# Optimization experiments

Measured on AMD Instinct MI355X. Metric: run time of the kernel, lower is better.

Reference implementation:

```python
import jax, jax.numpy as jnp
import numpy as np

NUM_GRAPHS = 256


def _gcn_norm(edge_index, num_nodes):
    # Add self-loops and compute symmetric normalization coeffs (PyG gcn_norm).
    loops = jnp.arange(num_nodes, dtype=edge_index.dtype)
    row = jnp.concatenate([edge_index[0], loops])  # source nodes
    col = jnp.concatenate([edge_index[1], loops])  # target nodes
    deg = jax.ops.segment_sum(jnp.ones_like(col, dtype=jnp.float32), col,
                              num_segments=num_nodes)
    dis = jnp.where(deg > 0, jax.lax.rsqrt(jnp.maximum(deg, 1.0)), 0.0)
    norm = dis[row] * dis[col]  # [E + N]
    return row, col, norm


def _gcn_conv(x, row, col, norm, W, b, num_nodes):
    h = x @ W                                        # [N, out] dense transform first
    msg = norm[:, None] * h[row]                     # gather + scale  [E+N, out]
    out = jax.ops.segment_sum(msg, col, num_segments=num_nodes)  # scatter-add
    return out + b


def setup_inputs() -> dict:
    key = jax.random.key(0)
    k = jax.random.split(key, 12)
    N, E, F_IN, H = 100000, 1600000, 64, 64
    x = jax.random.normal(k[0], (N, F_IN), dtype=jnp.float32)
    edge_index = jax.random.randint(k[1], (2, E), 0, N, dtype=jnp.int64)
    batch_index = jnp.sort(jax.random.randint(k[2], (N,), 0, NUM_GRAPHS, dtype=jnp.int64))
    s = 1.0 / np.sqrt(F_IN)
    W1 = jax.random.uniform(k[3], (F_IN, H), minval=-s, maxval=s, dtype=jnp.float32)
    b1 = jnp.zeros((H,), dtype=jnp.float32)
    W2 = jax.random.uniform(k[4], (H, H), minval=-s, maxval=s, dtype=jnp.float32)
    b2 = jnp.zeros((H,), dtype=jnp.float32)
    Wl1 = jax.random.uniform(k[5], (H, H // 2), minval=-s, maxval=s, dtype=jnp.float32)
    bl1 = jax.random.uniform(k[6], (H // 2,), minval=-s, maxval=s, dtype=jnp.float32)
    Wl2 = jax.random.uniform(k[7], (H // 2, 2), minval=-s, maxval=s, dtype=jnp.float32)
    bl2 = jax.random.uniform(k[8], (2,), minval=-s, maxval=s, dtype=jnp.float32)
    return {"x": x, "edge_index": edge_index, "batch_index": batch_index,
            "W1": W1, "b1": b1, "W2": W2, "b2": b2,
            "Wl1": Wl1, "bl1": bl1, "Wl2": Wl2, "bl2": bl2}


def reference(x, edge_index, batch_index, W1, b1, W2, b2, Wl1, bl1, Wl2, bl2):
    N = x.shape[0]
    row, col, norm = _gcn_norm(edge_index, N)
    h = jax.nn.relu(_gcn_conv(x, row, col, norm, W1, b1, N))
    h = jax.nn.relu(_gcn_conv(h, row, col, norm, W2, b2, N))
    # global mean pool over batch_index
    sums = jax.ops.segment_sum(h, batch_index, num_segments=NUM_GRAPHS)
    cnts = jax.ops.segment_sum(jnp.ones((N,), dtype=h.dtype), batch_index,
                               num_segments=NUM_GRAPHS)
    g = sums / jnp.maximum(cnts, 1.0)[:, None]       # [G, H]
    g = jax.nn.relu(g @ Wl1 + bl1)                    # dropout is identity in eval
    logits = g @ Wl2 + bl2
    return jax.nn.log_softmax(logits, axis=1)
```

## Files before the change

kernel.cpp:

```cpp
#include <hip/hip_runtime.h>
#include <hip/hip_fp8.h>
#include <cstdint>
#include <cstddef>


#define HF 64
#define BSH 8
#define BSZ 256
#define PCHUNK 4096
#define PADB 6144
#define CNTCLAMP (PADB - 4 * BSZ)
#define POISON 0xAAAAAAAAu

typedef unsigned u32;

__device__ __forceinline__ unsigned short f2bf(float x) {
    unsigned u = __float_as_uint(x);
    unsigned r = (u + 0x7fffu + ((u >> 16) & 1u)) >> 16;
    return (unsigned short)r;
}
__device__ __forceinline__ float bfl(u32 w) { return __uint_as_float(w << 16); }
__device__ __forceinline__ float bfh(u32 w) { return __uint_as_float(w & 0xffff0000u); }
__device__ __forceinline__ float bf2f(unsigned short s) { return __uint_as_float(((u32)s) << 16); }

__device__ __forceinline__ u32 pack_fp8x4(float a, float b, float c, float d) {
#if __has_builtin(__builtin_amdgcn_cvt_pk_fp8_f32)
    int v = 0;
    v = __builtin_amdgcn_cvt_pk_fp8_f32(a, b, v, false);
    v = __builtin_amdgcn_cvt_pk_fp8_f32(c, d, v, true);
    return (u32)v;
#else
    __hip_fp8_e4m3 fa(a), fb(b), fc(c), fd(d);
    return (u32)fa.__x | ((u32)fb.__x << 8) | ((u32)fc.__x << 16) | ((u32)fd.__x << 24);
#endif
}
__device__ __forceinline__ void acc_fp8x4(float4& acc, u32 w) {
#if __has_builtin(__builtin_amdgcn_cvt_pk_f32_fp8)
    typedef float v2f __attribute__((ext_vector_type(2)));
    v2f lo = __builtin_amdgcn_cvt_pk_f32_fp8((int)w, false);
    v2f hi = __builtin_amdgcn_cvt_pk_f32_fp8((int)w, true);
    acc.x += lo[0]; acc.y += lo[1]; acc.z += hi[0]; acc.w += hi[1];
#else
    __hip_fp8_e4m3 a, b, c, d;
    a.__x = (unsigned char)(w);       b.__x = (unsigned char)(w >> 8);
    c.__x = (unsigned char)(w >> 16); d.__x = (unsigned char)(w >> 24);
    acc.x += (float)a; acc.y += (float)b; acc.z += (float)c; acc.w += (float)d;
#endif
}

__global__ __launch_bounds__(256) void k_part(const int* __restrict__ rows,
                                              const int* __restrict__ cols,
                                              u32* __restrict__ gcurb,
                                              u32* __restrict__ part, int E) {
    __shared__ u32 hist[512];
    __shared__ u32 off[512];
    __shared__ u32 obase[512];
    __shared__ u32 cur[512];
    __shared__ u32 sc[256];
    __shared__ u32 stage[PCHUNK];
    __shared__ unsigned short sbk[PCHUNK];
    const int tid = threadIdx.x;
    const int e0  = blockIdx.x * PCHUNK;
    u32 er[16], ec[16];

    hist[tid] = 0; hist[tid + 256] = 0;
    __syncthreads();
#pragma unroll
    for (int j = 0; j < 16; ++j) {
        int e = e0 + j * 256 + tid;
        if (e < E) {
            ec[j] = (u32)cols[e];
            er[j] = (u32)rows[e];
            atomicAdd(&hist[ec[j] >> BSH], 1u);
        } else ec[j] = 0xFFFFFFFFu;
    }
    __syncthreads();
    u32 c0 = hist[2 * tid], c1 = hist[2 * tid + 1];
    u32 s = c0 + c1;
    sc[tid] = s;
    __syncthreads();
    for (int o = 1; o < 256; o <<= 1) {
        u32 t = (tid >= o) ? sc[tid - o] : 0u;
        __syncthreads();
        sc[tid] += t;
        __syncthreads();
    }
    u32 ex = sc[tid] - s;
    off[2 * tid] = ex;          cur[2 * tid] = ex;
    off[2 * tid + 1] = ex + c0; cur[2 * tid + 1] = ex + c0;
    obase[2 * tid]     = c0 ? (atomicAdd(&gcurb[2 * tid], c0) - POISON) : 0u;
    obase[2 * tid + 1] = c1 ? (atomicAdd(&gcurb[2 * tid + 1], c1) - POISON) : 0u;
    __syncthreads();
#pragma unroll
    for (int j = 0; j < 16; ++j) {
        if (ec[j] != 0xFFFFFFFFu) {
            u32 bk  = ec[j] >> BSH;
            u32 pos = atomicAdd(&cur[bk], 1u);
            stage[pos] = ((ec[j] & (BSZ - 1)) << 17) | er[j];
            sbk[pos]   = (unsigned short)bk;
        }
    }
    __syncthreads();
    const int total = (e0 + PCHUNK <= E) ? PCHUNK : (E - e0);
    for (int i = tid; i < total; i += 256) {
        u32 bk = sbk[i];
        u32 pb = obase[bk] + ((u32)i - off[bk]);
        if (pb < PADB)
            part[(size_t)bk * PADB + pb] = stage[i];
    }
}

__global__ __launch_bounds__(256) void k_place2(const u32* __restrict__ gcurb,
                                                const u32* __restrict__ part,
                                                const float* __restrict__ x,
                                                u32* __restrict__ rowptr,
                                                float* __restrict__ dis,
                                                u32* __restrict__ s08,
                                                int* __restrict__ eidx,
                                                int N, float S0) {
    __shared__ u32 cnt_[256];
    __shared__ u32 off_[257];
    __shared__ u32 sc[256];
    __shared__ u32 cur[256];
    __shared__ u32 outb[PADB];
    const int tid = threadIdx.x;
    const int b   = blockIdx.x;
    const int n0  = b << BSH;
    const u32 base = (u32)b * PADB;
    u32 cntB = gcurb[b] - POISON; if (cntB > CNTCLAMP) cntB = CNTCLAMP;

    if (b == 0 && tid < 16) s08[(size_t)N * 16 + tid] = 0u;

    cnt_[tid] = 0;
    __syncthreads();
    for (u32 i = tid; i < cntB; i += 256)
        atomicAdd(&cnt_[part[base + i] >> 17], 1u);
    __syncthreads();
    u32 v  = cnt_[tid];
    bool live = (n0 + tid) < N;
    u32 vs = v + 1u;
    u32 p  = live ? ((vs + 3u) & ~3u) : 0u;
    sc[tid] = p;
    __syncthreads();
    for (int o = 1; o < 256; o <<= 1) {
        u32 t = (tid >= o) ? sc[tid - o] : 0u;
        __syncthreads();
        sc[tid] += t;
        __syncthreads();
    }
    u32 ex = sc[tid] - p;
    off_[tid] = ex; cur[tid] = ex;
    if (tid == 255) off_[256] = sc[255];
    __syncthreads();
    const u32 cntP = off_[256];
    if (live) {
        u32 dg = vs; if (dg > 1023u) dg = 1023u;
        rowptr[n0 + tid] = (base + ex) | (dg << 22);
        dis[n0 + tid]    = rsqrtf(1.0f + (float)v);
    }
    {
        int nmax = min(256, N - n0);
        for (int idx = tid; idx < nmax * 16; idx += 256) {
            int nl = idx >> 4, f4 = idx & 15;
            float d  = S0 * rsqrtf(1.0f + (float)cnt_[nl]);
            float4 xv = ((const float4*)(x + (size_t)(n0 + nl) * HF))[f4];
            s08[(size_t)(n0 + nl) * 16 + f4] =
                pack_fp8x4(d * xv.x, d * xv.y, d * xv.z, d * xv.w);
        }
    }
    for (u32 i = tid; i < cntP; i += 256) outb[i] = (u32)N;
    __syncthreads();
    for (u32 i = tid; i < cntB; i += 256) {
        u32 pv  = part[base + i];
        u32 pos = atomicAdd(&cur[pv >> 17], 1u);
        outb[pos] = pv & 0x1FFFFu;
    }
    __syncthreads();
    if (live) outb[cur[tid]] = (u32)tid;
    __syncthreads();
    for (u32 i = tid; i < cntP; i += 256)
        eidx[base + i] = (int)outb[i];
}

__global__ __launch_bounds__(256) void k_gather(const u32* __restrict__ rowptr,
                                                const int* __restrict__ eidx,
                                                const u32* __restrict__ hs8,
                                                unsigned short* __restrict__ outbf,
                                                int N) {
    const int tid  = threadIdx.x;
    const int wv   = tid >> 6;
    const int lane = tid & 63;
    const int q    = lane >> 4;
    const int f4   = lane & 15;
    const int n    = blockIdx.x * 4 + wv;
    if (n >= N) return;

    u32 rp    = rowptr[n];
    u32 start = rp & 0x3FFFFFu;
    u32 deg   = rp >> 22;
    int ngr   = (int)((deg + 3u) >> 2);
    const uint4* eb = (const uint4*)(eidx + start);
    float4 acc = float4{0.f, 0.f, 0.f, 0.f};

    int g = q;
    for (; g + 4 < ngr; g += 8) {
        uint4 e4 = eb[g];
        uint4 e4b = eb[g + 4];
        u32 wa0 = hs8[(size_t)e4.x * 16 + f4];
        u32 wa1 = hs8[(size_t)e4.y * 16 + f4];
        u32 wa2 = hs8[(size_t)e4.z * 16 + f4];
        u32 wa3 = hs8[(size_t)e4.w * 16 + f4];
        u32 wb0 = hs8[(size_t)e4b.x * 16 + f4];
        u32 wb1 = hs8[(size_t)e4b.y * 16 + f4];
        u32 wb2 = hs8[(size_t)e4b.z * 16 + f4];
        u32 wb3 = hs8[(size_t)e4b.w * 16 + f4];
        acc_fp8x4(acc, wa0); acc_fp8x4(acc, wa1);
        acc_fp8x4(acc, wa2); acc_fp8x4(acc, wa3);
        acc_fp8x4(acc, wb0); acc_fp8x4(acc, wb1);
        acc_fp8x4(acc, wb2); acc_fp8x4(acc, wb3);
    }
    for (; g < ngr; g += 4) {
        uint4 e4 = eb[g];
        u32 w0 = hs8[(size_t)e4.x * 16 + f4];
        u32 w1 = hs8[(size_t)e4.y * 16 + f4];
        u32 w2 = hs8[(size_t)e4.z * 16 + f4];
        u32 w3 = hs8[(size_t)e4.w * 16 + f4];
        acc_fp8x4(acc, w0); acc_fp8x4(acc, w1);
        acc_fp8x4(acc, w2); acc_fp8x4(acc, w3);
    }
    acc.x += __shfl_xor(acc.x, 32); acc.y += __shfl_xor(acc.y, 32);
    acc.z += __shfl_xor(acc.z, 32); acc.w += __shfl_xor(acc.w, 32);
    acc.x += __shfl_xor(acc.x, 16); acc.y += __shfl_xor(acc.y, 16);
    acc.z += __shfl_xor(acc.z, 16); acc.w += __shfl_xor(acc.w, 16);

    if (q == 0) {
        ushort4 pk;
        pk.x = f2bf(acc.x); pk.y = f2bf(acc.y);
        pk.z = f2bf(acc.z); pk.w = f2bf(acc.w);
        *(ushort4*)&outbf[(size_t)n * HF + f4 * 4] = pk;
    }
}

template <int OUTFP8>
__global__ __launch_bounds__(256, 4) void k_trans(const unsigned short* __restrict__ T,
                                                  const float* __restrict__ W,
                                                  const float* __restrict__ dis,
                                                  const float* __restrict__ bias,
                                                  void* __restrict__ OUTp, int N,
                                                  float invS, float outS) {
    __shared__ float ws[64 * 64];
    __shared__ float xs[64 * 68];
    const int tid  = threadIdx.x;
    const int row0 = blockIdx.x * 64;

#pragma unroll
    for (int i = 0; i < 4; ++i) {
        int idx4 = i * 256 + tid;
        *(float4*)&ws[idx4 * 4] = ((const float4*)W)[idx4];
    }
#pragma unroll
    for (int i = 0; i < 4; ++i) {
        int idx4 = i * 256 + tid;
        int r    = idx4 >> 4;
        int kk   = (idx4 & 15) << 2;
        float4 v = float4{0.f, 0.f, 0.f, 0.f};
        int row  = row0 + r;
        if (row < N) {
            ushort4 pk = ((const ushort4*)(T + (size_t)row * HF))[idx4 & 15];
            v.x = bf2f(pk.x); v.y = bf2f(pk.y);
            v.z = bf2f(pk.z); v.w = bf2f(pk.w);
        }
        *(float4*)&xs[r * 68 + kk] = v;
    }
    __syncthreads();

    const int rg = tid >> 4;
    const int cg = tid & 15;
    float4 a0 = float4{0.f, 0.f, 0.f, 0.f};
    float4 a1 = a0, a2 = a0, a3 = a0;

#pragma unroll 8
    for (int k = 0; k < 64; ++k) {
        float4 wv = *(float4*)&ws[k * 64 + cg * 4];
        float  x0 = xs[(rg * 4 + 0) * 68 + k];
        float  x1 = xs[(rg * 4 + 1) * 68 + k];
        float  x2 = xs[(rg * 4 + 2) * 68 + k];
        float  x3 = xs[(rg * 4 + 3) * 68 + k];
        a0.x += x0 * wv.x; a0.y += x0 * wv.y; a0.z += x0 * wv.z; a0.w += x0 * wv.w;
        a1.x += x1 * wv.x; a1.y += x1 * wv.y; a1.z += x1 * wv.z; a1.w += x1 * wv.w;
        a2.x += x2 * wv.x; a2.y += x2 * wv.y; a2.z += x2 * wv.z; a2.w += x2 * wv.w;
        a3.x += x3 * wv.x; a3.y += x3 * wv.y; a3.z += x3 * wv.z; a3.w += x3 * wv.w;
    }

    float4 bv = ((const float4*)bias)[cg];
    float4 accs[4] = {a0, a1, a2, a3};
#pragma unroll
    for (int j = 0; j < 4; ++j) {
        int row = row0 + rg * 4 + j;
        if (row < N) {
            float d  = dis[row];
            float dd = d * invS;
            float4 a = accs[j];
            a.x = fmaxf(dd * a.x + bv.x, 0.f);
            a.y = fmaxf(dd * a.y + bv.y, 0.f);
            a.z = fmaxf(dd * a.z + bv.z, 0.f);
            a.w = fmaxf(dd * a.w + bv.w, 0.f);
            if (OUTFP8) {
                float so = d * outS;
                ((u32*)OUTp)[(size_t)row * 16 + cg] =
                    pack_fp8x4(so * a.x, so * a.y, so * a.z, so * a.w);
            } else {
                ushort4 pk;
                pk.x = f2bf(a.x); pk.y = f2bf(a.y);
                pk.z = f2bf(a.z); pk.w = f2bf(a.w);
                *(ushort4*)&((unsigned short*)OUTp)[(size_t)row * HF + cg * 4] = pk;
            }
        }
    }
}

__device__ __forceinline__ int lower_bound(const int* __restrict__ a, int n, int key) {
    int lo = 0, hi = n;
    while (lo < hi) { int mid = (lo + hi) >> 1; if (a[mid] < key) lo = mid + 1; else hi = mid; }
    return lo;
}

__global__ __launch_bounds__(256) void k_poolhead(const u32* __restrict__ h2,
                                                  const int* __restrict__ batch,
                                                  const float* __restrict__ Wl1,
                                                  const float* __restrict__ bl1,
                                                  const float* __restrict__ Wl2,
                                                  const float* __restrict__ bl2,
                                                  float* __restrict__ out, int N) {
    __shared__ float red[4][64];
    __shared__ float gm[64];
    const int g    = blockIdx.x;
    const int lane = threadIdx.x & 63;
    const int w    = threadIdx.x >> 6;
    int s = lower_bound(batch, N, g);
    int e = lower_bound(batch, N, g + 1);
    float acc = 0.f;
    for (int n = s + w; n < e; n += 4) {
        u32 wv = h2[(size_t)n * 32 + (lane >> 1)];
        acc += (lane & 1) ? bfh(wv) : bfl(wv);
    }
    red[w][lane] = acc;
    __syncthreads();
    if (w == 0) {
        float t = red[0][lane] + red[1][lane] + red[2][lane] + red[3][lane];
        gm[lane] = t / fmaxf((float)(e - s), 1.0f);
    }
    __syncthreads();
    if (w == 0 && lane < 32) {
        float a = bl1[lane];
#pragma unroll
        for (int k = 0; k < 64; ++k) a += gm[k] * Wl1[k * 32 + lane];
        a = fmaxf(a, 0.f);
        float l0 = a * Wl2[2 * lane];
        float l1 = a * Wl2[2 * lane + 1];
#pragma unroll
        for (int o = 1; o < 32; o <<= 1) {
            l0 += __shfl_xor(l0, o);
            l1 += __shfl_xor(l1, o);
        }
        if (lane == 0) {
            l0 += bl2[0]; l1 += bl2[1];
            float m   = fmaxf(l0, l1);
            float lse = m + logf(expf(l0 - m) + expf(l1 - m));
            out[2 * g]     = l0 - lse;
            out[2 * g + 1] = l1 - lse;
        }
    }
}

extern "C" void kernel_launch(void* const* d_in, const int* in_sizes, int n_in,
                              void* d_out, int out_size, void* d_ws, size_t ws_size,
                              hipStream_t stream) {
    const float* x   = (const float*)d_in[0];
    const int*   ei  = (const int*)d_in[1];
    const int*   bi  = (const int*)d_in[2];
    const float* W1  = (const float*)d_in[3];
    const float* b1  = (const float*)d_in[4];
    const float* W2  = (const float*)d_in[5];
    const float* b2  = (const float*)d_in[6];
    const float* Wl1 = (const float*)d_in[7];
    const float* bl1 = (const float*)d_in[8];
    const float* Wl2 = (const float*)d_in[9];
    const float* bl2 = (const float*)d_in[10];
    float* out = (float*)d_out;

    const int N = in_sizes[0] / HF;
    const int E = in_sizes[1] / 2;
    const int* rows = ei;
    const int* cols = ei + E;
    const int NB = (N + BSZ - 1) / BSZ;
    const size_t EP = (size_t)NB * PADB;

    const float S0 = 4.0f, S1 = 16.0f;

    float* ws = (float*)d_ws;
    size_t o = 0;
    float* dis    = ws + o; o += ((size_t)N + 63) / 64 * 64;
    u32*   RA     = (u32*)(ws + o); o += (size_t)(N + 1) * 32;
    unsigned short* RAh = (unsigned short*)RA;
    unsigned short* RB  = (unsigned short*)(ws + o); o += (size_t)(N + 1) * 32;
    u32*   rowptr = (u32*)(ws + o); o += ((size_t)N + 63) / 64 * 64;
    u32*   part   = (u32*)(ws + o); o += EP;
    int*   eidx   = (int*)(ws + o); o += EP;
    u32*   gcurb  = (u32*)(ws + o); o += 512;

    const int tb = (N + 63) / 64;

    k_part<<<(E + PCHUNK - 1) / PCHUNK, 256, 0, stream>>>(rows, cols, gcurb, part, E);
    k_place2<<<NB, 256, 0, stream>>>(gcurb, part, x, rowptr, dis, RA, eidx, N, S0);

    k_gather<<<(N + 3) / 4, 256, 0, stream>>>(rowptr, eidx, RA, RB, N);
    k_trans<1><<<tb, 256, 0, stream>>>(RB, W1, dis, b1, (void*)RA, N, 1.0f / S0, S1);
    k_gather<<<(N + 3) / 4, 256, 0, stream>>>(rowptr, eidx, RA, RB, N);
    k_trans<0><<<tb, 256, 0, stream>>>(RB, W2, dis, b2, (void*)RAh, N, 1.0f / S1, 0.f);

    k_poolhead<<<256, 256, 0, stream>>>((const u32*)RAh, bi, Wl1, bl1, Wl2, bl2, out, N);
}
```

Baseline: 277.6 us.

## Fuse neighbor gather into dense transform kernel, dropping bf16 intermediate

The separate gather kernel is merged into the transform kernel. Each block now gathers fp8 neighbor rows for its 64 nodes straight into shared memory and then applies W. This removes the bf16 round trip to global memory and one launch per layer. In exchange, each 16-lane group walks four nodes' edge lists one after another instead of one wave per node, so there is less memory-level parallelism per wave and the block is only as fast as its slowest node. Buffers are split into separate fp8 A/B arrays plus a bf16 output for pooling.

```diff
diff --git a/kernel.cpp b/kernel.cpp
--- a/kernel.cpp
+++ b/kernel.cpp
@@ -21,7 +21,6 @@
 }
 __device__ __forceinline__ float bfl(u32 w) { return __uint_as_float(w << 16); }
 __device__ __forceinline__ float bfh(u32 w) { return __uint_as_float(w & 0xffff0000u); }
-__device__ __forceinline__ float bf2f(unsigned short s) { return __uint_as_float(((u32)s) << 16); }
 
 __device__ __forceinline__ u32 pack_fp8x4(float a, float b, float c, float d) {
 #if __has_builtin(__builtin_amdgcn_cvt_pk_fp8_f32)
@@ -116,6 +115,7 @@
                                                 u32* __restrict__ rowptr,
                                                 float* __restrict__ dis,
                                                 u32* __restrict__ s08,
+                                                u32* __restrict__ h18,
                                                 int* __restrict__ eidx,
                                                 int N, float S0) {
     __shared__ u32 cnt_[256];
@@ -129,7 +129,10 @@
     const u32 base = (u32)b * PADB;
     u32 cntB = gcurb[b] - POISON; if (cntB > CNTCLAMP) cntB = CNTCLAMP;
 
-    if (b == 0 && tid < 16) s08[(size_t)N * 16 + tid] = 0u;
+    if (b == 0 && tid < 16) {
+        s08[(size_t)N * 16 + tid] = 0u;
+        h18[(size_t)N * 16 + tid] = 0u;
+    }
 
     cnt_[tid] = 0;
     __syncthreads();
@@ -182,72 +185,15 @@
         eidx[base + i] = (int)outb[i];
 }
 
-__global__ __launch_bounds__(256) void k_gather(const u32* __restrict__ rowptr,
-                                                const int* __restrict__ eidx,
-                                                const u32* __restrict__ hs8,
-                                                unsigned short* __restrict__ outbf,
-                                                int N) {
-    const int tid  = threadIdx.x;
-    const int wv   = tid >> 6;
-    const int lane = tid & 63;
-    const int q    = lane >> 4;
-    const int f4   = lane & 15;
-    const int n    = blockIdx.x * 4 + wv;
-    if (n >= N) return;
-
-    u32 rp    = rowptr[n];
-    u32 start = rp & 0x3FFFFFu;
-    u32 deg   = rp >> 22;
-    int ngr   = (int)((deg + 3u) >> 2);
-    const uint4* eb = (const uint4*)(eidx + start);
-    float4 acc = float4{0.f, 0.f, 0.f, 0.f};
-
-    int g = q;
-    for (; g + 4 < ngr; g += 8) {
-        uint4 e4 = eb[g];
-        uint4 e4b = eb[g + 4];
-        u32 wa0 = hs8[(size_t)e4.x * 16 + f4];
-        u32 wa1 = hs8[(size_t)e4.y * 16 + f4];
-        u32 wa2 = hs8[(size_t)e4.z * 16 + f4];
-        u32 wa3 = hs8[(size_t)e4.w * 16 + f4];
-        u32 wb0 = hs8[(size_t)e4b.x * 16 + f4];
-        u32 wb1 = hs8[(size_t)e4b.y * 16 + f4];
-        u32 wb2 = hs8[(size_t)e4b.z * 16 + f4];
-        u32 wb3 = hs8[(size_t)e4b.w * 16 + f4];
-        acc_fp8x4(acc, wa0); acc_fp8x4(acc, wa1);
-        acc_fp8x4(acc, wa2); acc_fp8x4(acc, wa3);
-        acc_fp8x4(acc, wb0); acc_fp8x4(acc, wb1);
-        acc_fp8x4(acc, wb2); acc_fp8x4(acc, wb3);
-    }
-    for (; g < ngr; g += 4) {
-        uint4 e4 = eb[g];
-        u32 w0 = hs8[(size_t)e4.x * 16 + f4];
-        u32 w1 = hs8[(size_t)e4.y * 16 + f4];
-        u32 w2 = hs8[(size_t)e4.z * 16 + f4];
-        u32 w3 = hs8[(size_t)e4.w * 16 + f4];
-        acc_fp8x4(acc, w0); acc_fp8x4(acc, w1);
-        acc_fp8x4(acc, w2); acc_fp8x4(acc, w3);
-    }
-    acc.x += __shfl_xor(acc.x, 32); acc.y += __shfl_xor(acc.y, 32);
-    acc.z += __shfl_xor(acc.z, 32); acc.w += __shfl_xor(acc.w, 32);
-    acc.x += __shfl_xor(acc.x, 16); acc.y += __shfl_xor(acc.y, 16);
-    acc.z += __shfl_xor(acc.z, 16); acc.w += __shfl_xor(acc.w, 16);
-
-    if (q == 0) {
-        ushort4 pk;
-        pk.x = f2bf(acc.x); pk.y = f2bf(acc.y);
-        pk.z = f2bf(acc.z); pk.w = f2bf(acc.w);
-        *(ushort4*)&outbf[(size_t)n * HF + f4 * 4] = pk;
-    }
-}
-
 template <int OUTFP8>
-__global__ __launch_bounds__(256, 4) void k_trans(const unsigned short* __restrict__ T,
-                                                  const float* __restrict__ W,
-                                                  const float* __restrict__ dis,
-                                                  const float* __restrict__ bias,
-                                                  void* __restrict__ OUTp, int N,
-                                                  float invS, float outS) {
+__global__ __launch_bounds__(256, 4) void k_gtrans(const u32* __restrict__ rowptr,
+                                                   const int* __restrict__ eidx,
+                                                   const u32* __restrict__ hs8,
+                                                   const float* __restrict__ W,
+                                                   const float* __restrict__ dis,
+                                                   const float* __restrict__ bias,
+                                                   void* __restrict__ OUTp, int N,
+                                                   float invS, float outS) {
     __shared__ float ws[64 * 64];
     __shared__ float xs[64 * 68];
     const int tid  = threadIdx.x;
@@ -258,19 +204,46 @@
         int idx4 = i * 256 + tid;
         *(float4*)&ws[idx4 * 4] = ((const float4*)W)[idx4];
     }
-#pragma unroll
-    for (int i = 0; i < 4; ++i) {
-        int idx4 = i * 256 + tid;
-        int r    = idx4 >> 4;
-        int kk   = (idx4 & 15) << 2;
-        float4 v = float4{0.f, 0.f, 0.f, 0.f};
-        int row  = row0 + r;
-        if (row < N) {
-            ushort4 pk = ((const ushort4*)(T + (size_t)row * HF))[idx4 & 15];
-            v.x = bf2f(pk.x); v.y = bf2f(pk.y);
-            v.z = bf2f(pk.z); v.w = bf2f(pk.w);
-        }
-        *(float4*)&xs[r * 68 + kk] = v;
+
+    const int qq = tid >> 4;
+    const int f4 = tid & 15;
+#pragma unroll 1
+    for (int j = 0; j < 4; ++j) {
+        const int n = row0 + qq * 4 + j;
+        float4 acc = float4{0.f, 0.f, 0.f, 0.f};
+        if (n < N) {
+            u32 rp    = rowptr[n];
+            u32 start = rp & 0x3FFFFFu;
+            int ngr   = (int)(((rp >> 22) + 3u) >> 2);
+            const uint4* eb = (const uint4*)(eidx + start);
+            int g = 0;
+            for (; g + 1 < ngr; g += 2) {
+                uint4 ea = eb[g];
+                uint4 eb2 = eb[g + 1];
+                u32 wa0 = hs8[(size_t)ea.x * 16 + f4];
+                u32 wa1 = hs8[(size_t)ea.y * 16 + f4];
+                u32 wa2 = hs8[(size_t)ea.z * 16 + f4];
+                u32 wa3 = hs8[(size_t)ea.w * 16 + f4];
+                u32 wb0 = hs8[(size_t)eb2.x * 16 + f4];
+                u32 wb1 = hs8[(size_t)eb2.y * 16 + f4];
+                u32 wb2 = hs8[(size_t)eb2.z * 16 + f4];
+                u32 wb3 = hs8[(size_t)eb2.w * 16 + f4];
+                acc_fp8x4(acc, wa0); acc_fp8x4(acc, wa1);
+                acc_fp8x4(acc, wa2); acc_fp8x4(acc, wa3);
+                acc_fp8x4(acc, wb0); acc_fp8x4(acc, wb1);
+                acc_fp8x4(acc, wb2); acc_fp8x4(acc, wb3);
+            }
+            if (g < ngr) {
+                uint4 ea = eb[g];
+                u32 w0 = hs8[(size_t)ea.x * 16 + f4];
+                u32 w1 = hs8[(size_t)ea.y * 16 + f4];
+                u32 w2 = hs8[(size_t)ea.z * 16 + f4];
+                u32 w3 = hs8[(size_t)ea.w * 16 + f4];
+                acc_fp8x4(acc, w0); acc_fp8x4(acc, w1);
+                acc_fp8x4(acc, w2); acc_fp8x4(acc, w3);
+            }
+        }
+        *(float4*)&xs[(qq * 4 + j) * 68 + f4 * 4] = acc;
     }
     __syncthreads();
 
@@ -401,9 +374,9 @@
     float* ws = (float*)d_ws;
     size_t o = 0;
     float* dis    = ws + o; o += ((size_t)N + 63) / 64 * 64;
-    u32*   RA     = (u32*)(ws + o); o += (size_t)(N + 1) * 32;
-    unsigned short* RAh = (unsigned short*)RA;
-    unsigned short* RB  = (unsigned short*)(ws + o); o += (size_t)(N + 1) * 32;
+    u32*   A8     = (u32*)(ws + o); o += (size_t)(N + 1) * 16;
+    u32*   B8     = (u32*)(ws + o); o += (size_t)(N + 1) * 16;
+    unsigned short* Cbf = (unsigned short*)(ws + o); o += (size_t)N * 32;
     u32*   rowptr = (u32*)(ws + o); o += ((size_t)N + 63) / 64 * 64;
     u32*   part   = (u32*)(ws + o); o += EP;
     int*   eidx   = (int*)(ws + o); o += EP;
@@ -412,12 +385,12 @@
     const int tb = (N + 63) / 64;
 
     k_part<<<(E + PCHUNK - 1) / PCHUNK, 256, 0, stream>>>(rows, cols, gcurb, part, E);
-    k_place2<<<NB, 256, 0, stream>>>(gcurb, part, x, rowptr, dis, RA, eidx, N, S0);
-
-    k_gather<<<(N + 3) / 4, 256, 0, stream>>>(rowptr, eidx, RA, RB, N);
-    k_trans<1><<<tb, 256, 0, stream>>>(RB, W1, dis, b1, (void*)RA, N, 1.0f / S0, S1);
-    k_gather<<<(N + 3) / 4, 256, 0, stream>>>(rowptr, eidx, RA, RB, N);
-    k_trans<0><<<tb, 256, 0, stream>>>(RB, W2, dis, b2, (void*)RAh, N, 1.0f / S1, 0.f);
-
-    k_poolhead<<<256, 256, 0, stream>>>((const u32*)RAh, bi, Wl1, bl1, Wl2, bl2, out, N);
-}
+    k_place2<<<NB, 256, 0, stream>>>(gcurb, part, x, rowptr, dis, A8, B8, eidx, N, S0);
+
+    k_gtrans<1><<<tb, 256, 0, stream>>>(rowptr, eidx, A8, W1, dis, b1, (void*)B8,
+                                        N, 1.0f / S0, S1);
+    k_gtrans<0><<<tb, 256, 0, stream>>>(rowptr, eidx, B8, W2, dis, b2, (void*)Cbf,
+                                        N, 1.0f / S1, 0.f);
+
+    k_poolhead<<<256, 256, 0, stream>>>((const u32*)Cbf, bi, Wl1, bl1, Wl2, bl2, out, N);
+}
```

After: 249.3 us. -10.2%, faster.
